# Kernel tuning notes

Measured on AMD Instinct MI355X. Metric: run time of the kernel, lower is better.

Reference implementation:

```python
import jax, jax.numpy as jnp
import numpy as np

NUM_EXPERTS = 8
HIDDEN = 1024
INTER = 2048
TOKENS = 2048
TOP_K = 2


def setup_inputs() -> dict:
    key = jax.random.key(0)
    k1, k2, k3, k4, k5 = jax.random.split(key, 5)
    hidden_states = jax.random.normal(k1, (TOKENS, HIDDEN), dtype=jnp.float32)
    top_k_index = jax.random.randint(k2, (TOKENS, TOP_K), 0, NUM_EXPERTS, dtype=jnp.int64)
    top_k_weights = jax.random.uniform(k3, (TOKENS, TOP_K), dtype=jnp.float32)
    # parameters, scaled like typical init
    gate_up_proj = jax.random.normal(k4, (NUM_EXPERTS, 2 * INTER, HIDDEN), dtype=jnp.float32) * (HIDDEN ** -0.5)
    down_proj = jax.random.normal(k5, (NUM_EXPERTS, HIDDEN, INTER), dtype=jnp.float32) * (INTER ** -0.5)
    return {
        "hidden_states": hidden_states,
        "top_k_index": top_k_index,
        "top_k_weights": top_k_weights,
        "gate_up_proj": gate_up_proj,
        "down_proj": down_proj,
    }


def reference(hidden_states, top_k_index, top_k_weights, gate_up_proj, down_proj):
    # combine weights per (token, expert): w[t, e] = sum_k 1[idx[t,k]==e] * tw[t,k]
    one_hot = jax.nn.one_hot(top_k_index, NUM_EXPERTS, dtype=hidden_states.dtype)  # [T, K, E]
    combine = jnp.einsum("tke,tk->te", one_hot, top_k_weights)  # [T, E]

    out = jnp.zeros_like(hidden_states)
    # fixed small loop over experts (structural, not a data dim)
    for e in range(NUM_EXPERTS):
        gu = hidden_states @ gate_up_proj[e].T  # [T, 2I]
        gate, up = jnp.split(gu, 2, axis=-1)
        h = jax.nn.gelu(gate, approximate=True) * up  # gelu_pytorch_tanh
        y = h @ down_proj[e].T  # [T, H]
        out = out + y * combine[:, e][:, None]
    return out
```

## Files before the change

### kernel.cpp

```cpp
#include <hip/hip_runtime.h>
#include <stdint.h>

#define T_TOK  2048
#define HID    1024
#define INTERN 2048
#define NEXP   8
#define MAXPOS 5248

typedef __attribute__((ext_vector_type(8))) short          bf16x8;
typedef __attribute__((ext_vector_type(4))) float          f32x4;
typedef __attribute__((ext_vector_type(8))) unsigned short u16x8;
typedef __attribute__((ext_vector_type(4))) unsigned short u16x4;

__device__ __forceinline__ unsigned short f32_to_bf16(float f) {
  unsigned int u = __float_as_uint(f);
  unsigned int r = (u + 0x7FFFu + ((u >> 16) & 1u)) >> 16;
  return (unsigned short)r;
}

__device__ __forceinline__ float bf16_to_f32(unsigned short h) {
  unsigned int u = ((unsigned int)h) << 16;
  return __uint_as_float(u);
}

__device__ __forceinline__ void gload_lds16(const void* g, void* l) {
  __builtin_amdgcn_global_load_lds(
      (const __attribute__((address_space(1))) unsigned int*)g,
      (__attribute__((address_space(3))) unsigned int*)l, 16, 0, 0);
}

__device__ __forceinline__ u16x8 cvt8(float4 a, float4 b) {
  union { u16x8 s; unsigned int u[4]; } r;
  asm("v_cvt_pk_bf16_f32 %0, %1, %2" : "=v"(r.u[0]) : "v"(a.x), "v"(a.y));
  asm("v_cvt_pk_bf16_f32 %0, %1, %2" : "=v"(r.u[1]) : "v"(a.z), "v"(a.w));
  asm("v_cvt_pk_bf16_f32 %0, %1, %2" : "=v"(r.u[2]) : "v"(b.x), "v"(b.y));
  asm("v_cvt_pk_bf16_f32 %0, %1, %2" : "=v"(r.u[3]) : "v"(b.z), "v"(b.w));
  return r.s;
}

#define WAIT_VM0()    asm volatile("s_waitcnt vmcnt(0)" ::: "memory")
#define WAIT_VM4()    asm volatile("s_waitcnt vmcnt(4)" ::: "memory")
#define WAIT_LGKM0()  asm volatile("s_waitcnt lgkmcnt(0)" ::: "memory")
#define SCHED_FENCE() __builtin_amdgcn_sched_barrier(0)

__global__ void route_kernel(const int* __restrict__ tki,
                             const float* __restrict__ tkw,
                             int* __restrict__ counts,
                             int* __restrict__ offsets,
                             int* __restrict__ tok_list,
                             float* __restrict__ w_list,
                             int* __restrict__ pos_map,
                             float* __restrict__ wgt_map) {
  __shared__ int scnt[NEXP];
  __shared__ int soff[NEXP];
  int tid = threadIdx.x;
  if (tid < NEXP) scnt[tid] = 0;
  __syncthreads();
  for (int t = tid; t < T_TOK; t += 256) {
    int e0 = tki[2 * t] & 7;
    int e1 = tki[2 * t + 1] & 7;
    float w0 = tkw[2 * t];
    float w1 = tkw[2 * t + 1];
    if (e0 == e1) {
      int p = atomicAdd(&scnt[e0], 1);
      tok_list[e0 * T_TOK + p] = t;
      w_list [e0 * T_TOK + p] = w0 + w1;
      pos_map[2 * t]     = (p << 3) | e0;
      wgt_map[2 * t]     = w0 + w1;
      pos_map[2 * t + 1] = -1;
      wgt_map[2 * t + 1] = 0.0f;
    } else {
      int p = atomicAdd(&scnt[e0], 1);
      tok_list[e0 * T_TOK + p] = t;
      w_list [e0 * T_TOK + p] = w0;
      pos_map[2 * t]     = (p << 3) | e0;
      wgt_map[2 * t]     = w0;
      int q = atomicAdd(&scnt[e1], 1);
      tok_list[e1 * T_TOK + q] = t;
      w_list [e1 * T_TOK + q] = w1;
      pos_map[2 * t + 1] = (q << 3) | e1;
      wgt_map[2 * t + 1] = w1;
    }
  }
  __syncthreads();
  if (tid == 0) {
    int acc = 0;
    for (int e = 0; e < NEXP; ++e) {
      counts[e]  = scnt[e];
      offsets[e] = acc;
      soff[e]    = acc;
      acc += ((scnt[e] + 127) >> 7) << 7;
    }
  }
  __syncthreads();
  for (int i = tid; i < 2 * T_TOK; i += 256) {
    int v = pos_map[i];
    if (v >= 0) pos_map[i] = soff[v & 7] + (v >> 3);
  }
}

__global__ void gather_cvt_x_kernel(const float* __restrict__ hidden,
                                    const int* __restrict__ counts,
                                    const int* __restrict__ offsets,
                                    const int* __restrict__ tok_list,
                                    unsigned short* __restrict__ xg) {
  int p = blockIdx.x * 2 + (threadIdx.x >> 7);
  int c = threadIdx.x & 127;
  int e = 0;
#pragma unroll
  for (int k = 1; k < NEXP; ++k) if (p >= offsets[k]) e = k;
  int r = p - offsets[e];
  float4 a = {0.f, 0.f, 0.f, 0.f}, b = {0.f, 0.f, 0.f, 0.f};
  if (r < counts[e]) {
    int tok = tok_list[e * T_TOK + r];
    const float4* src = (const float4*)(hidden + (size_t)tok * HID + c * 8);
    a = src[0]; b = src[1];
  }
  *((u16x8*)(xg + (size_t)(p >> 7) * 131072 + c * 1024 + (p & 127) * 8)) = cvt8(a, b);
}

__global__ __launch_bounds__(256, 4)
void gemm1_kernel(const unsigned short* __restrict__ xg,
                  const float* __restrict__ gup,
                  const int* __restrict__ counts,
                  const int* __restrict__ offsets,
                  unsigned short* __restrict__ hbuf) {
  int e  = blockIdx.z;
  int Ne = counts[e];
  int m0 = blockIdx.y * 128;
  if (m0 >= Ne) return;
  int n0  = blockIdx.x * 64;
  int off = offsets[e];

  __shared__ __align__(16) unsigned short As[2][4][128][8];
  __shared__ __align__(16) unsigned short Gs[2][4][64][8];
  __shared__ __align__(16) unsigned short Us[2][4][64][8];

  int tid  = threadIdx.x;
  int lane = tid & 63;
  int wave = tid >> 6;
  int wm = wave >> 1;
  int wn = wave & 1;

  const unsigned short* asrc = xg + (size_t)((off + m0) >> 7) * (HID * 128);

  int brow = tid >> 2;
  int bq   = tid & 3;
  const float* gsrc = gup + (size_t)e * (2 * INTERN) * HID + (size_t)(n0 + brow) * HID + bq * 8;
  const float* usrc = gsrc + (size_t)INTERN * HID;
  int brw = brow ^ bq;

  f32x4 accg[4][2], accu[4][2];
#pragma unroll
  for (int m = 0; m < 4; ++m)
#pragma unroll
    for (int n = 0; n < 2; ++n) {
      accg[m][n] = (f32x4){0.f, 0.f, 0.f, 0.f};
      accu[m][n] = (f32x4){0.f, 0.f, 0.f, 0.f};
    }

  float4 g0, g1, u0, u1;

  {
    char* base = (char*)&As[0][0][0][0];
    gload_lds16(asrc + (size_t)tid * 8,        base + (size_t)tid * 16);
    gload_lds16(asrc + 2048 + (size_t)tid * 8, base + 4096 + (size_t)tid * 16);
    const float4* gp = (const float4*)gsrc;
    const float4* up = (const float4*)usrc;
    float4 tg0 = gp[0], tg1 = gp[1], tu0 = up[0], tu1 = up[1];
    *((u16x8*)&Gs[0][bq][brw][0]) = cvt8(tg0, tg1);
    *((u16x8*)&Us[0][bq][brw][0]) = cvt8(tu0, tu1);
    const float4* gp1 = (const float4*)(gsrc + 32);
    const float4* up1 = (const float4*)(usrc + 32);
    g0 = gp1[0]; g1 = gp1[1]; u0 = up1[0]; u1 = up1[1];
    WAIT_LGKM0(); SCHED_FENCE();
  }

  int cur = 0;
  const int NT = HID / 32;
  for (int t = 0; t < NT; ++t) {
    WAIT_VM4(); SCHED_FENCE();
    __builtin_amdgcn_s_barrier(); SCHED_FENCE();
    int nxt = cur ^ 1;
    int ka = (t + 1 < NT) ? (t + 1) * 32 : 0;
    {
      char* base = (char*)&As[nxt][0][0][0];
      const unsigned short* ak = asrc + (size_t)ka * 128;
      gload_lds16(ak + (size_t)tid * 8,        base + (size_t)tid * 16);
      gload_lds16(ak + 2048 + (size_t)tid * 8, base + 4096 + (size_t)tid * 16);
    }
    SCHED_FENCE();
    {
      int kg = lane >> 4;
      int rl = lane & 15;
      bf16x8 af[4], gf[2], uf[2];
#pragma unroll
      for (int m = 0; m < 4; ++m)
        af[m] = *((const bf16x8*)&As[cur][kg][wm * 64 + m * 16 + rl][0]);
#pragma unroll
      for (int n = 0; n < 2; ++n) {
        int r = (wn * 32 + n * 16 + rl) ^ kg;
        gf[n] = *((const bf16x8*)&Gs[cur][kg][r][0]);
        uf[n] = *((const bf16x8*)&Us[cur][kg][r][0]);
      }
#pragma unroll
      for (int m = 0; m < 4; ++m)
#pragma unroll
        for (int n = 0; n < 2; ++n) {
          accg[m][n] = __builtin_amdgcn_mfma_f32_16x16x32_bf16(af[m], gf[n], accg[m][n], 0, 0, 0);
          accu[m][n] = __builtin_amdgcn_mfma_f32_16x16x32_bf16(af[m], uf[n], accu[m][n], 0, 0, 0);
        }
    }
    *((u16x8*)&Gs[nxt][bq][brw][0]) = cvt8(g0, g1);
    *((u16x8*)&Us[nxt][bq][brw][0]) = cvt8(u0, u1);
    SCHED_FENCE();
    {
      int kb = (t + 2 < NT) ? (t + 2) * 32 : 0;
      const float4* gp = (const float4*)(gsrc + kb);
      const float4* up = (const float4*)(usrc + kb);
      g0 = gp[0]; g1 = gp[1]; u0 = up[0]; u1 = up[1];
    }
    WAIT_LGKM0(); SCHED_FENCE();
    cur = nxt;
  }
  WAIT_VM0();

  int rl = lane & 15;
  int rq = lane >> 4;
  size_t hb_base = (size_t)((off + m0) >> 7) * (INTERN * 128);
#pragma unroll
  for (int m = 0; m < 4; ++m) {
#pragma unroll
    for (int n = 0; n < 2; ++n) {
      int col = n0 + wn * 32 + n * 16 + rl;
      size_t cbase = hb_base + (size_t)(col >> 3) * 1024 + (col & 7);
#pragma unroll
      for (int j = 0; j < 4; ++j) {
        int lr = wm * 64 + m * 16 + rq * 4 + j;
        if (m0 + lr < Ne) {
          float gv = accg[m][n][j];
          float uv = accu[m][n][j];
          float tt2 = gv + 0.044715f * gv * gv * gv;
          float a  = gv / (1.0f + __expf(-1.5957691216f * tt2));
          hbuf[cbase + (size_t)lr * 8] = f32_to_bf16(a * uv);
        }
      }
    }
  }
}

__global__ __launch_bounds__(256, 2)
void gemm2_kernel(const unsigned short* __restrict__ hbuf,
                  const float* __restrict__ down,
                  const int* __restrict__ counts,
                  const int* __restrict__ offsets,
                  unsigned short* __restrict__ ybuf) {
  int e  = blockIdx.z;
  int Ne = counts[e];
  int m0 = blockIdx.y * 128;
  if (m0 >= Ne) return;
  int n0  = blockIdx.x * 64;
  int off = offsets[e];

  __shared__ __align__(16) unsigned short As[2][8][128][8];
  __shared__ __align__(16) unsigned short Bs[2][8][64][8];

  int tid  = threadIdx.x;
  int lane = tid & 63;
  int wave = tid >> 6;
  int wm = wave >> 1;
  int wn = wave & 1;

  const unsigned short* asrc = hbuf + (size_t)((off + m0) >> 7) * (INTERN * 128);

  int brow = tid >> 2;
  int bq   = tid & 3;
  int kgw0 = bq * 2, kgw1 = bq * 2 + 1;
  const float* bsrc = down + (size_t)e * HID * INTERN + (size_t)(n0 + brow) * INTERN + bq * 16;

  f32x4 acc[4][2];
#pragma unroll
  for (int m = 0; m < 4; ++m)
#pragma unroll
    for (int n = 0; n < 2; ++n) acc[m][n] = (f32x4){0.f, 0.f, 0.f, 0.f};

  float4 b0, b1, b2, b3;

  {
    char* base = (char*)&As[0][0][0][0];
#pragma unroll
    for (int o = 0; o < 4; ++o)
      gload_lds16(asrc + o * 2048 + (size_t)tid * 8, base + o * 4096 + (size_t)tid * 16);
    const float4* bp = (const float4*)bsrc;
    float4 t0 = bp[0], t1 = bp[1], t2 = bp[2], t3 = bp[3];
    *((u16x8*)&Bs[0][kgw0][brow ^ kgw0][0]) = cvt8(t0, t1);
    *((u16x8*)&Bs[0][kgw1][brow ^ kgw1][0]) = cvt8(t2, t3);
    const float4* bp1 = (const float4*)(bsrc + 64);
    b0 = bp1[0]; b1 = bp1[1]; b2 = bp1[2]; b3 = bp1[3];
    WAIT_LGKM0(); SCHED_FENCE();
  }

  int cur = 0;
  const int NT = INTERN / 64;
  for (int t = 0; t < NT; ++t) {
    WAIT_VM4(); SCHED_FENCE();
    __builtin_amdgcn_s_barrier(); SCHED_FENCE();
    int nxt = cur ^ 1;
    int ka = (t + 1 < NT) ? (t + 1) * 64 : 0;
    {
      char* base = (char*)&As[nxt][0][0][0];
      const unsigned short* ak = asrc + (size_t)ka * 128;
#pragma unroll
      for (int o = 0; o < 4; ++o)
        gload_lds16(ak + o * 2048 + (size_t)tid * 8, base + o * 4096 + (size_t)tid * 16);
    }
    SCHED_FENCE();
#pragma unroll
    for (int kk = 0; kk < 2; ++kk) {
      int kg = kk * 4 + (lane >> 4);
      int rl = lane & 15;
      bf16x8 af[4], bfv[2];
#pragma unroll
      for (int m = 0; m < 4; ++m)
        af[m] = *((const bf16x8*)&As[cur][kg][wm * 64 + m * 16 + rl][0]);
#pragma unroll
      for (int n = 0; n < 2; ++n)
        bfv[n] = *((const bf16x8*)&Bs[cur][kg][(wn * 32 + n * 16 + rl) ^ kg][0]);
#pragma unroll
      for (int m = 0; m < 4; ++m)
#pragma unroll
        for (int n = 0; n < 2; ++n)
          acc[m][n] = __builtin_amdgcn_mfma_f32_16x16x32_bf16(af[m], bfv[n], acc[m][n], 0, 0, 0);
    }
    *((u16x8*)&Bs[nxt][kgw0][brow ^ kgw0][0]) = cvt8(b0, b1);
    *((u16x8*)&Bs[nxt][kgw1][brow ^ kgw1][0]) = cvt8(b2, b3);
    SCHED_FENCE();
    {
      int kb = (t + 2 < NT) ? (t + 2) * 64 : 0;
      const float4* bp = (const float4*)(bsrc + kb);
      b0 = bp[0]; b1 = bp[1]; b2 = bp[2]; b3 = bp[3];
    }
    WAIT_LGKM0(); SCHED_FENCE();
    cur = nxt;
  }
  WAIT_VM0();

  int rl = lane & 15;
  int rq = lane >> 4;
#pragma unroll
  for (int m = 0; m < 4; ++m) {
#pragma unroll
    for (int n = 0; n < 2; ++n) {
      int col = n0 + wn * 32 + n * 16 + rl;
#pragma unroll
      for (int j = 0; j < 4; ++j) {
        int lr = wm * 64 + m * 16 + rq * 4 + j;
        if (m0 + lr < Ne)
          ybuf[(size_t)(off + m0 + lr) * HID + col] = f32_to_bf16(acc[m][n][j]);
      }
    }
  }
}

__global__ void combine_kernel(const int* __restrict__ pos_map,
                               const float* __restrict__ wgt_map,
                               const unsigned short* __restrict__ ybuf,
                               float* __restrict__ out) {
  int i  = blockIdx.x * 256 + threadIdx.x;
  int t  = i >> 7;
  int c8 = i & 127;
  int p0 = pos_map[2 * t];
  int p1 = pos_map[2 * t + 1];
  float w0 = wgt_map[2 * t];
  float w1 = wgt_map[2 * t + 1];
  float acc[8];
#pragma unroll
  for (int j = 0; j < 8; ++j) acc[j] = 0.f;
  if (p0 >= 0) {
    u16x8 v = *((const u16x8*)(ybuf + (size_t)p0 * HID + c8 * 8));
#pragma unroll
    for (int j = 0; j < 8; ++j) acc[j] += w0 * bf16_to_f32(v[j]);
  }
  if (p1 >= 0) {
    u16x8 v = *((const u16x8*)(ybuf + (size_t)p1 * HID + c8 * 8));
#pragma unroll
    for (int j = 0; j < 8; ++j) acc[j] += w1 * bf16_to_f32(v[j]);
  }
  float4 o0 = make_float4(acc[0], acc[1], acc[2], acc[3]);
  float4 o1 = make_float4(acc[4], acc[5], acc[6], acc[7]);
  float4* dst = (float4*)(out + (size_t)t * HID + c8 * 8);
  dst[0] = o0;
  dst[1] = o1;
}

extern "C" void kernel_launch(void* const* d_in, const int* in_sizes, int n_in,
                              void* d_out, int out_size, void* d_ws, size_t ws_size,
                              hipStream_t stream) {
  (void)in_sizes; (void)n_in; (void)out_size;
  const float* hidden = (const float*)d_in[0];
  const int*   tki    = (const int*)d_in[1];
  const float* tkw    = (const float*)d_in[2];
  const float* gup    = (const float*)d_in[3];
  const float* down   = (const float*)d_in[4];
  float* out = (float*)d_out;
  char*  ws  = (char*)d_ws;

  int*   counts   = (int*)  (ws + 0);
  int*   offsets  = (int*)  (ws + 64);
  int*   tok_list = (int*)  (ws + 256);
  int*   pos_map  = (int*)  (ws + 65792);
  float* wgt_map  = (float*)(ws + 82176);
  float* w_list   = (float*)(ws + 98560);
  unsigned short* hbuf = (unsigned short*)(ws + 4358400);
  unsigned short* ybuf = (unsigned short*)(ws + 25854208);
  unsigned short* xg   = ybuf;

  if (ws_size < 36602112ull) return;

  hipLaunchKernelGGL(route_kernel, dim3(1), dim3(256), 0, stream,
                     tki, tkw, counts, offsets, tok_list, w_list, pos_map, wgt_map);
  hipLaunchKernelGGL(gather_cvt_x_kernel, dim3(MAXPOS / 2), dim3(256), 0, stream,
                     hidden, counts, offsets, tok_list, xg);
  hipLaunchKernelGGL(gemm1_kernel, dim3(INTERN / 64, T_TOK / 128, NEXP), dim3(256), 0, stream,
                     xg, gup, counts, offsets, hbuf);
  hipLaunchKernelGGL(gemm2_kernel, dim3(HID / 64, T_TOK / 128, NEXP), dim3(256), 0, stream,
                     hbuf, down, counts, offsets, ybuf);
  hipLaunchKernelGGL(combine_kernel, dim3(T_TOK * HID / 8 / 256), dim3(256), 0, stream,
                     pos_map, wgt_map, ybuf, out);
}
```

Baseline: 139.3 us.

## Pre-convert gate_up weights to tiled bf16 and use a triple-buffered bf16 GEMM1

Adds a kernel that converts the fp32 gate_up weights on every call into bf16, laid out in 64-row, K-grouped tiles that match the LDS fragment layout. A new GEMM1 kernel then streams these tiles, together with the activations, straight into LDS with a three-stage buffer and fuses the gelu*up epilogue. The goal is to drop the in-loop fp32 weight conversion and halve the weight bytes reloaded by each M-block. In exchange, it adds a full read and write pass over the 128MB weight tensor on every call, and the path only runs when the workspace is large enough.

Result: slower. 176.9 us (+27.0%).

```diff
diff --git a/kernel.cpp b/kernel.cpp
--- a/kernel.cpp
+++ b/kernel.cpp
@@ -119,12 +119,146 @@
   *((u16x8*)(xg + (size_t)(p >> 7) * 131072 + c * 1024 + (p & 127) * 8)) = cvt8(a, b);
 }
 
+__global__ void cvt_w_kernel(const float* __restrict__ gup,
+                             unsigned short* __restrict__ wgb) {
+  __shared__ float T[64][129];
+  int ks = blockIdx.x;
+  int pr = blockIdx.y;
+  int e  = blockIdx.z;
+  int tid = threadIdx.x;
+  const float* src = gup + ((size_t)e * 4096 + (size_t)pr * 64) * 1024 + ks * 128;
+  for (int i = tid; i < 2048; i += 256) {
+    int r  = i >> 5;
+    int c4 = i & 31;
+    float4 v = *((const float4*)(src + (size_t)r * 1024 + c4 * 4));
+    T[r][c4 * 4 + 0] = v.x; T[r][c4 * 4 + 1] = v.y;
+    T[r][c4 * 4 + 2] = v.z; T[r][c4 * 4 + 3] = v.w;
+  }
+  __syncthreads();
+  unsigned short* dst = wgb + (size_t)(e * 64 + pr) * 65536 + (size_t)ks * 16 * 512;
+  for (int j = tid; j < 1024; j += 256) {
+    int kg = j >> 6;
+    int r  = j & 63;
+    float4 a = make_float4(T[r][kg * 8 + 0], T[r][kg * 8 + 1], T[r][kg * 8 + 2], T[r][kg * 8 + 3]);
+    float4 b = make_float4(T[r][kg * 8 + 4], T[r][kg * 8 + 5], T[r][kg * 8 + 6], T[r][kg * 8 + 7]);
+    *((u16x8*)(dst + (size_t)kg * 512 + r * 8)) = cvt8(a, b);
+  }
+}
+
+__global__ __launch_bounds__(256, 3)
+void gemm1_bf16_kernel(const unsigned short* __restrict__ xg,
+                       const unsigned short* __restrict__ wgb,
+                       const int* __restrict__ counts,
+                       const int* __restrict__ offsets,
+                       unsigned short* __restrict__ hbuf) {
+  int e  = blockIdx.z;
+  int Ne = counts[e];
+  int m0 = blockIdx.y * 128;
+  if (m0 >= Ne) return;
+  int nb = blockIdx.x;
+  int n0 = nb * 64;
+  int off = offsets[e];
+
+  __shared__ __align__(16) unsigned short As[3][4][128][8];
+  __shared__ __align__(16) unsigned short Gs[3][4][64][8];
+  __shared__ __align__(16) unsigned short Us[3][4][64][8];
+
+  int tid  = threadIdx.x;
+  int lane = tid & 63;
+  int wave = tid >> 6;
+  int wm = wave >> 1;
+  int wn = wave & 1;
+  int kg4 = lane >> 4;
+  int rl  = lane & 15;
+
+  const unsigned short* abase = xg + (size_t)((off + m0) >> 7) * (HID * 128);
+  const unsigned short* gP = wgb + (size_t)(e * 64 + nb) * 65536;
+  const unsigned short* uP = wgb + (size_t)(e * 64 + 32 + nb) * 65536;
+
+  f32x4 accg[4][2], accu[4][2];
+#pragma unroll
+  for (int m = 0; m < 4; ++m)
+#pragma unroll
+    for (int n = 0; n < 2; ++n) {
+      accg[m][n] = (f32x4){0.f, 0.f, 0.f, 0.f};
+      accu[m][n] = (f32x4){0.f, 0.f, 0.f, 0.f};
+    }
+
+  const int NT = HID / 32;
+
+#define G1DMA(BUF, T)                                                                   \
+  {                                                                                     \
+    int tt_ = ((T) < NT) ? (T) : 0;                                                     \
+    const unsigned short* a_ = abase + (size_t)tt_ * 4096;                              \
+    gload_lds16(a_ + (size_t)tid * 8,        (char*)&As[BUF][0][0][0] + (size_t)tid * 16); \
+    gload_lds16(a_ + 2048 + (size_t)tid * 8, (char*)&As[BUF][0][0][0] + 4096 + (size_t)tid * 16); \
+    gload_lds16(gP + (size_t)tt_ * 2048 + (size_t)tid * 8, (char*)&Gs[BUF][0][0][0] + (size_t)tid * 16); \
+    gload_lds16(uP + (size_t)tt_ * 2048 + (size_t)tid * 8, (char*)&Us[BUF][0][0][0] + (size_t)tid * 16); \
+  }
+
+  G1DMA(0, 0);
+  G1DMA(1, 1);
+  WAIT_VM4(); SCHED_FENCE();
+  __builtin_amdgcn_s_barrier(); SCHED_FENCE();
+
+  for (int t = 0; t < NT; ++t) {
+    int cb  = t % 3;
+    int pb  = (t + 2) % 3;
+    G1DMA(pb, t + 2);
+    SCHED_FENCE();
+    {
+      bf16x8 af[4], gf[2], uf[2];
+#pragma unroll
+      for (int m = 0; m < 4; ++m)
+        af[m] = *((const bf16x8*)&As[cb][kg4][wm * 64 + m * 16 + rl][0]);
+#pragma unroll
+      for (int n = 0; n < 2; ++n) {
+        gf[n] = *((const bf16x8*)&Gs[cb][kg4][wn * 32 + n * 16 + rl][0]);
+        uf[n] = *((const bf16x8*)&Us[cb][kg4][wn * 32 + n * 16 + rl][0]);
+      }
+#pragma unroll
+      for (int m = 0; m < 4; ++m)
+#pragma unroll
+        for (int n = 0; n < 2; ++n) {
+          accg[m][n] = __builtin_amdgcn_mfma_f32_16x16x32_bf16(af[m], gf[n], accg[m][n], 0, 0, 0);
+          accu[m][n] = __builtin_amdgcn_mfma_f32_16x16x32_bf16(af[m], uf[n], accu[m][n], 0, 0, 0);
+        }
+    }
+    WAIT_VM4(); SCHED_FENCE();
+    __builtin_amdgcn_s_barrier(); SCHED_FENCE();
+  }
+  WAIT_VM0();
+#undef G1DMA
+
+  int rq = lane >> 4;
+  size_t hb_base = (size_t)((off + m0) >> 7) * (INTERN * 128);
+#pragma unroll
+  for (int m = 0; m < 4; ++m) {
+#pragma unroll
+    for (int n = 0; n < 2; ++n) {
+      int col = n0 + wn * 32 + n * 16 + rl;
+      size_t cbase = hb_base + (size_t)(col >> 3) * 1024 + (col & 7);
+#pragma unroll
+      for (int j = 0; j < 4; ++j) {
+        int lr = wm * 64 + m * 16 + rq * 4 + j;
+        if (m0 + lr < Ne) {
+          float gv = accg[m][n][j];
+          float uv = accu[m][n][j];
+          float tt2 = gv + 0.044715f * gv * gv * gv;
+          float a  = gv / (1.0f + __expf(-1.5957691216f * tt2));
+          hbuf[cbase + (size_t)lr * 8] = f32_to_bf16(a * uv);
+        }
+      }
+    }
+  }
+}
+
 __global__ __launch_bounds__(256, 4)
-void gemm1_kernel(const unsigned short* __restrict__ xg,
-                  const float* __restrict__ gup,
-                  const int* __restrict__ counts,
-                  const int* __restrict__ offsets,
-                  unsigned short* __restrict__ hbuf) {
+void gemm1_f32_kernel(const unsigned short* __restrict__ xg,
+                      const float* __restrict__ gup,
+                      const int* __restrict__ counts,
+                      const int* __restrict__ offsets,
+                      unsigned short* __restrict__ hbuf) {
   int e  = blockIdx.z;
   int Ne = counts[e];
   int m0 = blockIdx.y * 128;
@@ -414,15 +548,23 @@
   unsigned short* hbuf = (unsigned short*)(ws + 4358400);
   unsigned short* ybuf = (unsigned short*)(ws + 25854208);
   unsigned short* xg   = ybuf;
+  unsigned short* wgb  = (unsigned short*)(ws + 36602112);
 
   if (ws_size < 36602112ull) return;
+  int big = (ws_size >= 103710976ull);
 
   hipLaunchKernelGGL(route_kernel, dim3(1), dim3(256), 0, stream,
                      tki, tkw, counts, offsets, tok_list, w_list, pos_map, wgt_map);
   hipLaunchKernelGGL(gather_cvt_x_kernel, dim3(MAXPOS / 2), dim3(256), 0, stream,
                      hidden, counts, offsets, tok_list, xg);
-  hipLaunchKernelGGL(gemm1_kernel, dim3(INTERN / 64, T_TOK / 128, NEXP), dim3(256), 0, stream,
-                     xg, gup, counts, offsets, hbuf);
+  if (big) {
+    hipLaunchKernelGGL(cvt_w_kernel, dim3(8, 64, NEXP), dim3(256), 0, stream, gup, wgb);
+    hipLaunchKernelGGL(gemm1_bf16_kernel, dim3(INTERN / 64, T_TOK / 128, NEXP), dim3(256), 0, stream,
+                       xg, wgb, counts, offsets, hbuf);
+  } else {
+    hipLaunchKernelGGL(gemm1_f32_kernel, dim3(INTERN / 64, T_TOK / 128, NEXP), dim3(256), 0, stream,
+                       xg, gup, counts, offsets, hbuf);
+  }
   hipLaunchKernelGGL(gemm2_kernel, dim3(HID / 64, T_TOK / 128, NEXP), dim3(256), 0, stream,
                      hbuf, down, counts, offsets, ybuf);
   hipLaunchKernelGGL(combine_kernel, dim3(T_TOK * HID / 8 / 256), dim3(256), 0, stream,
```

## Split gate/up GEMM into two passes with gate intermediate buffer

Applied to the files above, without the earlier changes.

Replaces the fused gate+up GEMM1 with two launches: the first computes the gate projection into a bf16 scratch buffer, the second computes the up projection and applies GELU-tanh times up using the stored gate values. Each pass uses a single B tile with a larger K-chunk of 64 and lower occupancy bounds, aiming to cut per-block LDS and register pressure. It adds an extra write and read of the gate intermediate plus a second launch. It only takes effect when the workspace is large enough, otherwise the fused kernel is kept.

Result: slower. 183.0 us (+31.4%).

```diff
diff --git a/kernel.cpp b/kernel.cpp
--- a/kernel.cpp
+++ b/kernel.cpp
@@ -119,12 +119,141 @@
   *((u16x8*)(xg + (size_t)(p >> 7) * 131072 + c * 1024 + (p & 127) * 8)) = cvt8(a, b);
 }
 
+template <int UP>
+__global__ __launch_bounds__(256, 2)
+void gemm1_half_kernel(const unsigned short* __restrict__ xg,
+                       const float* __restrict__ gup,
+                       const int* __restrict__ counts,
+                       const int* __restrict__ offsets,
+                       unsigned short* __restrict__ gbuf,
+                       unsigned short* __restrict__ hbuf) {
+  int e  = blockIdx.z;
+  int Ne = counts[e];
+  int m0 = blockIdx.y * 128;
+  if (m0 >= Ne) return;
+  int n0  = blockIdx.x * 64;
+  int off = offsets[e];
+
+  __shared__ __align__(16) unsigned short As[2][8][128][8];
+  __shared__ __align__(16) unsigned short Bs[2][8][64][8];
+
+  int tid  = threadIdx.x;
+  int lane = tid & 63;
+  int wave = tid >> 6;
+  int wm = wave >> 1;
+  int wn = wave & 1;
+
+  const unsigned short* asrc = xg + (size_t)((off + m0) >> 7) * (HID * 128);
+
+  int brow = tid >> 2;
+  int bq   = tid & 3;
+  int kgw0 = bq * 2, kgw1 = bq * 2 + 1;
+  const float* bsrc = gup + (size_t)e * (2 * INTERN) * HID
+                    + (size_t)(UP ? INTERN : 0) * HID
+                    + (size_t)(n0 + brow) * HID + bq * 16;
+
+  f32x4 acc[4][2];
+#pragma unroll
+  for (int m = 0; m < 4; ++m)
+#pragma unroll
+    for (int n = 0; n < 2; ++n) acc[m][n] = (f32x4){0.f, 0.f, 0.f, 0.f};
+
+  float4 b0, b1, b2, b3;
+
+  {
+    char* base = (char*)&As[0][0][0][0];
+#pragma unroll
+    for (int o = 0; o < 4; ++o)
+      gload_lds16(asrc + o * 2048 + (size_t)tid * 8, base + o * 4096 + (size_t)tid * 16);
+    const float4* bp = (const float4*)bsrc;
+    float4 t0 = bp[0], t1 = bp[1], t2 = bp[2], t3 = bp[3];
+    *((u16x8*)&Bs[0][kgw0][brow ^ kgw0][0]) = cvt8(t0, t1);
+    *((u16x8*)&Bs[0][kgw1][brow ^ kgw1][0]) = cvt8(t2, t3);
+    const float4* bp1 = (const float4*)(bsrc + 64);
+    b0 = bp1[0]; b1 = bp1[1]; b2 = bp1[2]; b3 = bp1[3];
+    WAIT_LGKM0(); SCHED_FENCE();
+  }
+
+  int cur = 0;
+  const int NT = HID / 64;
+  for (int t = 0; t < NT; ++t) {
+    WAIT_VM4(); SCHED_FENCE();
+    __builtin_amdgcn_s_barrier(); SCHED_FENCE();
+    int nxt = cur ^ 1;
+    int ka = (t + 1 < NT) ? (t + 1) * 64 : 0;
+    {
+      char* base = (char*)&As[nxt][0][0][0];
+      const unsigned short* ak = asrc + (size_t)ka * 128;
+#pragma unroll
+      for (int o = 0; o < 4; ++o)
+        gload_lds16(ak + o * 2048 + (size_t)tid * 8, base + o * 4096 + (size_t)tid * 16);
+    }
+    SCHED_FENCE();
+#pragma unroll
+    for (int kk = 0; kk < 2; ++kk) {
+      int kg = kk * 4 + (lane >> 4);
+      int rl = lane & 15;
+      bf16x8 af[4], bfv[2];
+#pragma unroll
+      for (int m = 0; m < 4; ++m)
+        af[m] = *((const bf16x8*)&As[cur][kg][wm * 64 + m * 16 + rl][0]);
+#pragma unroll
+      for (int n = 0; n < 2; ++n)
+        bfv[n] = *((const bf16x8*)&Bs[cur][kg][(wn * 32 + n * 16 + rl) ^ kg][0]);
+#pragma unroll
+      for (int m = 0; m < 4; ++m)
+#pragma unroll
+        for (int n = 0; n < 2; ++n)
+          acc[m][n] = __builtin_amdgcn_mfma_f32_16x16x32_bf16(af[m], bfv[n], acc[m][n], 0, 0, 0);
+    }
+    *((u16x8*)&Bs[nxt][kgw0][brow ^ kgw0][0]) = cvt8(b0, b1);
+    *((u16x8*)&Bs[nxt][kgw1][brow ^ kgw1][0]) = cvt8(b2, b3);
+    SCHED_FENCE();
+    {
+      int kb = (t + 2 < NT) ? (t + 2) * 64 : 0;
+      const float4* bp = (const float4*)(bsrc + kb);
+      b0 = bp[0]; b1 = bp[1]; b2 = bp[2]; b3 = bp[3];
+    }
+    WAIT_LGKM0(); SCHED_FENCE();
+    cur = nxt;
+  }
+  WAIT_VM0();
+
+  int rl = lane & 15;
+  int rq = lane >> 4;
+  size_t hb_base = (size_t)((off + m0) >> 7) * (INTERN * 128);
+#pragma unroll
+  for (int m = 0; m < 4; ++m) {
+#pragma unroll
+    for (int n = 0; n < 2; ++n) {
+      int col = n0 + wn * 32 + n * 16 + rl;
+      size_t cbase = hb_base + (size_t)(col >> 3) * 1024 + (col & 7);
+#pragma unroll
+      for (int j = 0; j < 4; ++j) {
+        int lr = wm * 64 + m * 16 + rq * 4 + j;
+        if (m0 + lr < Ne) {
+          size_t idx = cbase + (size_t)lr * 8;
+          if (UP) {
+            float gv = bf16_to_f32(gbuf[idx]);
+            float uv = acc[m][n][j];
+            float tt2 = gv + 0.044715f * gv * gv * gv;
+            float a  = gv / (1.0f + __expf(-1.5957691216f * tt2));
+            hbuf[idx] = f32_to_bf16(a * uv);
+          } else {
+            gbuf[idx] = f32_to_bf16(acc[m][n][j]);
+          }
+        }
+      }
+    }
+  }
+}
+
 __global__ __launch_bounds__(256, 4)
-void gemm1_kernel(const unsigned short* __restrict__ xg,
-                  const float* __restrict__ gup,
-                  const int* __restrict__ counts,
-                  const int* __restrict__ offsets,
-                  unsigned short* __restrict__ hbuf) {
+void gemm1_fused_kernel(const unsigned short* __restrict__ xg,
+                        const float* __restrict__ gup,
+                        const int* __restrict__ counts,
+                        const int* __restrict__ offsets,
+                        unsigned short* __restrict__ hbuf) {
   int e  = blockIdx.z;
   int Ne = counts[e];
   int m0 = blockIdx.y * 128;
@@ -414,15 +543,24 @@
   unsigned short* hbuf = (unsigned short*)(ws + 4358400);
   unsigned short* ybuf = (unsigned short*)(ws + 25854208);
   unsigned short* xg   = ybuf;
+  unsigned short* gbuf = (unsigned short*)(ws + 36602112);
 
   if (ws_size < 36602112ull) return;
+  int split = (ws_size >= 58097920ull);
 
   hipLaunchKernelGGL(route_kernel, dim3(1), dim3(256), 0, stream,
                      tki, tkw, counts, offsets, tok_list, w_list, pos_map, wgt_map);
   hipLaunchKernelGGL(gather_cvt_x_kernel, dim3(MAXPOS / 2), dim3(256), 0, stream,
                      hidden, counts, offsets, tok_list, xg);
-  hipLaunchKernelGGL(gemm1_kernel, dim3(INTERN / 64, T_TOK / 128, NEXP), dim3(256), 0, stream,
-                     xg, gup, counts, offsets, hbuf);
+  if (split) {
+    hipLaunchKernelGGL((gemm1_half_kernel<0>), dim3(INTERN / 64, T_TOK / 128, NEXP), dim3(256), 0, stream,
+                       xg, gup, counts, offsets, gbuf, hbuf);
+    hipLaunchKernelGGL((gemm1_half_kernel<1>), dim3(INTERN / 64, T_TOK / 128, NEXP), dim3(256), 0, stream,
+                       xg, gup, counts, offsets, gbuf, hbuf);
+  } else {
+    hipLaunchKernelGGL(gemm1_fused_kernel, dim3(INTERN / 64, T_TOK / 128, NEXP), dim3(256), 0, stream,
+                       xg, gup, counts, offsets, hbuf);
+  }
   hipLaunchKernelGGL(gemm2_kernel, dim3(HID / 64, T_TOK / 128, NEXP), dim3(256), 0, stream,
                      hbuf, down, counts, offsets, ybuf);
   hipLaunchKernelGGL(combine_kernel, dim3(T_TOK * HID / 8 / 256), dim3(256), 0, stream,
```
